# Performance work log

Measured on AMD Instinct MI355X. Metric: run time of the kernel, lower is better.

The kernel has to match this reference:

```python
import jax, jax.numpy as jnp
import numpy as np

N, L, D = 4, 2048, 1024
H_DIM, OUT_DIM = 1024, 1024


def setup_inputs() -> dict:
    key = jax.random.key(0)
    ks = jax.random.split(key, 7)
    scale = 0.02
    return {
        "x": jax.random.normal(ks[0], (N, L, D), dtype=jnp.float32),
        "Wq": jax.random.normal(ks[1], (D, H_DIM), dtype=jnp.float32) * scale,
        "bq": jnp.zeros((H_DIM,), dtype=jnp.float32),
        "Wk": jax.random.normal(ks[2], (D, H_DIM), dtype=jnp.float32) * scale,
        "bk": jnp.zeros((H_DIM,), dtype=jnp.float32),
        "Wv": jax.random.normal(ks[3], (D, OUT_DIM), dtype=jnp.float32) * scale,
        "bv": jnp.zeros((OUT_DIM,), dtype=jnp.float32),
    }


def reference(x, Wq, bq, Wk, bk, Wv, bv):
    # q,k: [N,L,h_dim], v: [N,L,out_dim]
    q = jnp.einsum("nld,dh->nlh", x, Wq) + bq
    k = jnp.einsum("nld,dh->nlh", x, Wk) + bk
    v = jnp.einsum("nld,do->nlo", x, Wv) + bv
    # scores: [N,L,L]
    qk = jnp.einsum("nlh,nmh->nlm", q, k)
    # NOTE: original scales by sqrt(qk.shape[-1]) == sqrt(L) (seq len), not sqrt(h_dim)
    seq_len = qk.shape[-1]
    s = jax.nn.softmax(qk / jnp.sqrt(jnp.asarray(seq_len, dtype=qk.dtype)), axis=-1)
    return jnp.einsum("nlm,nmo->nlo", s, v)
```

## Files before the change

### kernel.cpp

```cpp
#include <hip/hip_runtime.h>
#include <hip/hip_bf16.h>


typedef __attribute__((ext_vector_type(8))) short bf16x8;
typedef __attribute__((ext_vector_type(4))) float f32x4;

#define AS_G(p) ((__attribute__((address_space(1))) void*)(p))
#define AS_L(p) ((__attribute__((address_space(3))) void*)(p))

__device__ __forceinline__ unsigned short f2bf(float f) {
  unsigned int u = __float_as_uint(f);
  unsigned int lsb = (u >> 16) & 1u;
  u += 0x7fffu + lsb;
  return (unsigned short)(u >> 16);
}

__device__ __forceinline__ float bf2f(unsigned short h) {
  return __uint_as_float(((unsigned int)h) << 16);
}


template <int EPI>
__global__ __launch_bounds__(256) void gemm64(
    const unsigned short* __restrict__ A, const unsigned short* __restrict__ B,
    float* __restrict__ Cf, long long sA, long long sB, long long sC,
    int K, int lda, int ldb, int ldc,
    unsigned short* __restrict__ u0, unsigned short* __restrict__ u1,
    unsigned short* __restrict__ u2,
    const float* __restrict__ f0, const float* __restrict__ f1,
    const float* __restrict__ f2,
    float* __restrict__ rsum, float scale)
{
  __shared__ unsigned short lA[128 * 64];
  __shared__ unsigned short lB[128 * 64];

  const int t = threadIdx.x;
  const int rowBase = blockIdx.y * 128;
  const int colBase = blockIdx.x * 128;
  A += (long long)blockIdx.z * sA;
  B += (long long)blockIdx.z * sB;

  const int l = t & 63;
  const int w = t >> 6;
  const int wrow = (w >> 1) * 64;
  const int wcol = (w & 1) * 64;
  const int q = l >> 4;
  const int r16 = l & 15;

  f32x4 acc[4][4] = {};

  const int r0 = t >> 3;
  const int goff = (((t & 7) ^ (r0 & 7)) << 3);

  for (int kt = 0; kt < K; kt += 64) {
    __syncthreads();
#pragma unroll
    for (int u = 0; u < 4; u++) {
      const int row = r0 + 32 * u;
      __builtin_amdgcn_global_load_lds(AS_G(A + (size_t)(rowBase + row) * lda + kt + goff),
                                       AS_L(lA + (t + 256 * u) * 8), 16, 0, 0);
      __builtin_amdgcn_global_load_lds(AS_G(B + (size_t)(colBase + row) * ldb + kt + goff),
                                       AS_L(lB + (t + 256 * u) * 8), 16, 0, 0);
    }
    __syncthreads();

#pragma unroll
    for (int ks = 0; ks < 2; ks++) {
      bf16x8 af[4], bfr[4];
#pragma unroll
      for (int i = 0; i < 4; i++) {
        const int s = ((ks * 4 + q) ^ (r16 & 7));
        af[i] = *(const bf16x8*)(lA + (wrow + i * 16 + r16) * 64 + s * 8);
      }
#pragma unroll
      for (int j = 0; j < 4; j++) {
        const int s = ((ks * 4 + q) ^ (r16 & 7));
        bfr[j] = *(const bf16x8*)(lB + (wcol + j * 16 + r16) * 64 + s * 8);
      }
#pragma unroll
      for (int i = 0; i < 4; i++)
#pragma unroll
        for (int j = 0; j < 4; j++)
          acc[i][j] = __builtin_amdgcn_mfma_f32_16x16x32_bf16(af[i], bfr[j], acc[i][j], 0, 0, 0);
    }
  }

  if (EPI == 1) {
    unsigned short* p16 = u0 + (long long)blockIdx.z * sC;
    float* rs = rsum + (long long)blockIdx.z * 2048;
#pragma unroll
    for (int i = 0; i < 4; i++) {
#pragma unroll
      for (int r = 0; r < 4; r++) {
        int row = rowBase + wrow + i * 16 + q * 4 + r;
        float rowpart = 0.f;
#pragma unroll
        for (int j = 0; j < 4; j++) {
          int col = colBase + wcol + j * 16 + r16;
          float e = __expf(acc[i][j][r] * scale);
          p16[(size_t)row * ldc + col] = f2bf(e);
          rowpart += e;
        }
#pragma unroll
        for (int m = 1; m < 16; m <<= 1) rowpart += __shfl_xor(rowpart, m);
        if (r16 == 0) atomicAdd(rs + row, rowpart);
      }
    }
  } else if (EPI == 2) {
    const int seg = colBase >> 10;
    if (seg < 2) {
      unsigned short* dst = seg ? u1 : u0;
      const float* bias = seg ? f1 : f0;
      const int cb = colBase & 1023;
#pragma unroll
      for (int i = 0; i < 4; i++) {
#pragma unroll
        for (int r = 0; r < 4; r++) {
          int row = rowBase + wrow + i * 16 + q * 4 + r;
#pragma unroll
          for (int j = 0; j < 4; j++) {
            int col = cb + wcol + j * 16 + r16;
            dst[(size_t)row * 1024 + col] = f2bf(acc[i][j][r] + bias[col]);
          }
        }
      }
    } else {
      const int ob = colBase - 2048;
#pragma unroll
      for (int i = 0; i < 4; i++) {
        int posBase = rowBase + wrow + i * 16 + q * 4;
        int b = posBase >> 11;
        int pos = posBase & 2047;
#pragma unroll
        for (int j = 0; j < 4; j++) {
          int o = ob + wcol + j * 16 + r16;
          float bias = f2[o];
          ushort4 pk;
          pk.x = f2bf(acc[i][j][0] + bias);
          pk.y = f2bf(acc[i][j][1] + bias);
          pk.z = f2bf(acc[i][j][2] + bias);
          pk.w = f2bf(acc[i][j][3] + bias);
          *(ushort4*)(u2 + ((size_t)((b << 10) + o) * 2048 + pos)) = pk;
        }
      }
    }
  } else {
    float* C = Cf + (long long)blockIdx.z * sC;
    const float* rs = rsum + (long long)blockIdx.z * 2048;
#pragma unroll
    for (int i = 0; i < 4; i++) {
#pragma unroll
      for (int r = 0; r < 4; r++) {
        int row = rowBase + wrow + i * 16 + q * 4 + r;
        float inv = 1.0f / rs[row];
#pragma unroll
        for (int j = 0; j < 4; j++) {
          int col = colBase + wcol + j * 16 + r16;
          C[(size_t)row * ldc + col] = acc[i][j][r] * inv;
        }
      }
    }
  }
}


__global__ __launch_bounds__(256) void cast_f32_to_bf16(
    const float* __restrict__ in, unsigned short* __restrict__ out, int n4,
    float* __restrict__ rzero, int nz4)
{
  int i = blockIdx.x * 256 + threadIdx.x;
  if (i < nz4) ((float4*)rzero)[i] = make_float4(0.f, 0.f, 0.f, 0.f);
  if (i >= n4) return;
  float4 v = ((const float4*)in)[i];
  ushort4 o;
  o.x = f2bf(v.x); o.y = f2bf(v.y); o.z = f2bf(v.z); o.w = f2bf(v.w);
  ((ushort4*)out)[i] = o;
}


__global__ __launch_bounds__(256) void wtrans(
    const float* __restrict__ Wq, const float* __restrict__ Wk,
    const float* __restrict__ Wv, unsigned short* __restrict__ WT)
{
  __shared__ float tile[32][33];
  const float* in = blockIdx.z == 0 ? Wq : (blockIdx.z == 1 ? Wk : Wv);
  unsigned short* out = WT + (size_t)blockIdx.z * 1024 * 1024;
  const int bc = blockIdx.x * 32;
  const int br = blockIdx.y * 32;
  const int tx = threadIdx.x;
  const int ty = threadIdx.y;
#pragma unroll
  for (int i = 0; i < 4; i++)
    tile[ty + i * 8][tx] = in[(size_t)(br + ty + i * 8) * 1024 + bc + tx];
  __syncthreads();
#pragma unroll
  for (int i = 0; i < 4; i++)
    out[(size_t)(bc + ty + i * 8) * 1024 + br + tx] = f2bf(tile[tx][ty + i * 8]);
}


extern "C" void kernel_launch(void* const* d_in, const int* in_sizes, int n_in,
                              void* d_out, int out_size, void* d_ws, size_t ws_size,
                              hipStream_t stream) {
  (void)in_sizes; (void)n_in; (void)out_size;

  const float* x  = (const float*)d_in[0];
  const float* Wq = (const float*)d_in[1];
  const float* bq = (const float*)d_in[2];
  const float* Wk = (const float*)d_in[3];
  const float* bk = (const float*)d_in[4];
  const float* Wv = (const float*)d_in[5];
  const float* bv = (const float*)d_in[6];
  float* out = (float*)d_out;

  const int Nb = 4, L = 2048, D = 1024, H = 1024, O = 1024;
  const int M = Nb * L;
  const int NQKV = 3 * H;

  char* ws = (char*)d_ws;
  size_t off = 0;
  unsigned short* xb = (unsigned short*)(ws + off); off += (size_t)M * D * 2;
  unsigned short* qb = (unsigned short*)(ws + off); off += (size_t)M * H * 2;
  unsigned short* kb = (unsigned short*)(ws + off); off += (size_t)M * H * 2;
  unsigned short* vt = (unsigned short*)(ws + off); off += (size_t)M * O * 2;
  unsigned short* WT = (unsigned short*)(ws + off); off += (size_t)NQKV * D * 2;
  unsigned short* P  = (unsigned short*)(ws + off); off += (size_t)Nb * L * L * 2;
  float* rsum = (float*)(ws + off); off += (size_t)Nb * L * 4;
  if (ws_size < off) return;

  dim3 blk256(256);

  cast_f32_to_bf16<<<(M * D / 4 + 255) / 256, blk256, 0, stream>>>(
      x, xb, M * D / 4, rsum, Nb * L / 4);

  wtrans<<<dim3(32, 32, 3), dim3(32, 8), 0, stream>>>(Wq, Wk, Wv, WT);

  gemm64<2><<<dim3(NQKV / 128, M / 128, 1), blk256, 0, stream>>>(
      xb, WT, nullptr, 0, 0, 0, D, D, D, 0,
      qb, kb, vt, bq, bk, bv, nullptr, 0.f);

  gemm64<1><<<dim3(L / 128, L / 128, Nb), blk256, 0, stream>>>(
      qb, kb, nullptr, (long long)L * H, (long long)L * H, (long long)L * L,
      H, H, H, L,
      P, nullptr, nullptr, nullptr, nullptr, nullptr,
      rsum, 0.022097086912079608f );

  gemm64<3><<<dim3(O / 128, L / 128, Nb), blk256, 0, stream>>>(
      P, vt, out, (long long)L * L, (long long)O * L, (long long)L * O,
      L, L, L, O,
      nullptr, nullptr, nullptr, nullptr, nullptr, nullptr,
      rsum, 0.f);
}
```

Before: 264.1 us.

## Triple-buffer GEMM LDS loads and enlarge tiles to 256x128 with 512 threads

Replaces the single-buffered GEMM with a three-stage LDS pipeline that prefetches two K-tiles ahead using async global-to-LDS loads and vmcnt waits. Tiles grow to 256x128 per block with 8 waves, all fragment reads are hoisted before the MFMA burst, and wave priority is raised during the MFMAs. The aim is to hide global load latency and cut per-tile barrier stalls. In exchange it uses about 144KB of LDS per block, which limits occupancy, and it relies on correct manual waitcnt accounting.

```diff
diff --git a/kernel.cpp b/kernel.cpp
--- a/kernel.cpp
+++ b/kernel.cpp
@@ -15,13 +15,28 @@
   return (unsigned short)(u >> 16);
 }
 
-__device__ __forceinline__ float bf2f(unsigned short h) {
-  return __uint_as_float(((unsigned int)h) << 16);
-}
-
+#define WAITV(n) asm volatile("s_waitcnt vmcnt(" #n ")" ::: "memory")
+#define WAITL0   asm volatile("s_waitcnt lgkmcnt(0)" ::: "memory")
+#define BARRIER() do { __builtin_amdgcn_s_barrier(); asm volatile("" ::: "memory"); } while (0)
+
+
+#define STAGE(ktk, bb) do {                                                          \
+    unsigned short* dA_ = lds + (bb) * 24576;                                        \
+    unsigned short* dB_ = dA_ + 16384;                                               \
+    _Pragma("unroll")                                                                \
+    for (int u_ = 0; u_ < 4; u_++)                                                   \
+      __builtin_amdgcn_global_load_lds(                                              \
+          AS_G(A + (size_t)(rowBase + r0 + 64 * u_) * lda + (ktk) + goff),           \
+          AS_L(dA_ + ((size_t)t + 512 * u_) * 8), 16, 0, 0);                         \
+    _Pragma("unroll")                                                                \
+    for (int u_ = 0; u_ < 2; u_++)                                                   \
+      __builtin_amdgcn_global_load_lds(                                              \
+          AS_G(B + (size_t)(colBase + r0 + 64 * u_) * ldb + (ktk) + goff),           \
+          AS_L(dB_ + ((size_t)t + 512 * u_) * 8), 16, 0, 0);                         \
+  } while (0)
 
 template <int EPI>
-__global__ __launch_bounds__(256) void gemm64(
+__global__ __launch_bounds__(512, 2) void gemm_pipe(
     const unsigned short* __restrict__ A, const unsigned short* __restrict__ B,
     float* __restrict__ Cf, long long sA, long long sB, long long sC,
     int K, int lda, int ldb, int ldc,
@@ -31,11 +46,10 @@
     const float* __restrict__ f2,
     float* __restrict__ rsum, float scale)
 {
-  __shared__ unsigned short lA[128 * 64];
-  __shared__ unsigned short lB[128 * 64];
+  __shared__ unsigned short lds[3 * 24576];
 
   const int t = threadIdx.x;
-  const int rowBase = blockIdx.y * 128;
+  const int rowBase = blockIdx.y * 256;
   const int colBase = blockIdx.x * 128;
   A += (long long)blockIdx.z * sA;
   B += (long long)blockIdx.z * sB;
@@ -47,42 +61,55 @@
   const int q = l >> 4;
   const int r16 = l & 15;
 
+  const int r0 = t >> 3;
+  const int goff = ((t & 7) ^ (r0 & 7)) << 3;
+
   f32x4 acc[4][4] = {};
 
-  const int r0 = t >> 3;
-  const int goff = (((t & 7) ^ (r0 & 7)) << 3);
-
-  for (int kt = 0; kt < K; kt += 64) {
-    __syncthreads();
-#pragma unroll
-    for (int u = 0; u < 4; u++) {
-      const int row = r0 + 32 * u;
-      __builtin_amdgcn_global_load_lds(AS_G(A + (size_t)(rowBase + row) * lda + kt + goff),
-                                       AS_L(lA + (t + 256 * u) * 8), 16, 0, 0);
-      __builtin_amdgcn_global_load_lds(AS_G(B + (size_t)(colBase + row) * ldb + kt + goff),
-                                       AS_L(lB + (t + 256 * u) * 8), 16, 0, 0);
-    }
-    __syncthreads();
-
+  const int NT = K >> 6;
+
+  STAGE(0, 0);
+  STAGE(64, 1);
+
+  int cur = 0;
+  for (int it = 0; it < NT; ++it) {
+    const int kt = it << 6;
+    if (it + 2 < NT) {
+      int b2 = cur + 2; if (b2 >= 3) b2 -= 3;
+      STAGE(kt + 128, b2);
+      WAITV(12);
+    } else if (it + 1 < NT) {
+      WAITV(6);
+    } else {
+      WAITV(0);
+    }
+    BARRIER();
+
+    const unsigned short* bufA = lds + cur * 24576;
+    const unsigned short* bufB = bufA + 16384;
+    bf16x8 af[2][4], bfr[2][4];
 #pragma unroll
     for (int ks = 0; ks < 2; ks++) {
-      bf16x8 af[4], bfr[4];
-#pragma unroll
-      for (int i = 0; i < 4; i++) {
-        const int s = ((ks * 4 + q) ^ (r16 & 7));
-        af[i] = *(const bf16x8*)(lA + (wrow + i * 16 + r16) * 64 + s * 8);
-      }
-#pragma unroll
-      for (int j = 0; j < 4; j++) {
-        const int s = ((ks * 4 + q) ^ (r16 & 7));
-        bfr[j] = *(const bf16x8*)(lB + (wcol + j * 16 + r16) * 64 + s * 8);
-      }
+      const int s = (((ks * 4 + q) ^ (r16 & 7)) << 3);
 #pragma unroll
       for (int i = 0; i < 4; i++)
+        af[ks][i] = *(const bf16x8*)(bufA + (wrow + i * 16 + r16) * 64 + s);
+#pragma unroll
+      for (int j = 0; j < 4; j++)
+        bfr[ks][j] = *(const bf16x8*)(bufB + (wcol + j * 16 + r16) * 64 + s);
+    }
+    __builtin_amdgcn_s_setprio(1);
+#pragma unroll
+    for (int ks = 0; ks < 2; ks++)
+#pragma unroll
+      for (int i = 0; i < 4; i++)
 #pragma unroll
         for (int j = 0; j < 4; j++)
-          acc[i][j] = __builtin_amdgcn_mfma_f32_16x16x32_bf16(af[i], bfr[j], acc[i][j], 0, 0, 0);
-    }
+          acc[i][j] = __builtin_amdgcn_mfma_f32_16x16x32_bf16(af[ks][i], bfr[ks][j], acc[i][j], 0, 0, 0);
+    __builtin_amdgcn_s_setprio(0);
+    WAITL0;
+    BARRIER();
+    cur++; if (cur >= 3) cur -= 3;
   }
 
   if (EPI == 1) {
@@ -229,23 +256,24 @@
   if (ws_size < off) return;
 
   dim3 blk256(256);
+  dim3 blk512(512);
 
   cast_f32_to_bf16<<<(M * D / 4 + 255) / 256, blk256, 0, stream>>>(
       x, xb, M * D / 4, rsum, Nb * L / 4);
 
   wtrans<<<dim3(32, 32, 3), dim3(32, 8), 0, stream>>>(Wq, Wk, Wv, WT);
 
-  gemm64<2><<<dim3(NQKV / 128, M / 128, 1), blk256, 0, stream>>>(
+  gemm_pipe<2><<<dim3(NQKV / 128, M / 256, 1), blk512, 0, stream>>>(
       xb, WT, nullptr, 0, 0, 0, D, D, D, 0,
       qb, kb, vt, bq, bk, bv, nullptr, 0.f);
 
-  gemm64<1><<<dim3(L / 128, L / 128, Nb), blk256, 0, stream>>>(
+  gemm_pipe<1><<<dim3(L / 128, L / 256, Nb), blk512, 0, stream>>>(
       qb, kb, nullptr, (long long)L * H, (long long)L * H, (long long)L * L,
       H, H, H, L,
       P, nullptr, nullptr, nullptr, nullptr, nullptr,
       rsum, 0.022097086912079608f );
 
-  gemm64<3><<<dim3(O / 128, L / 128, Nb), blk256, 0, stream>>>(
+  gemm_pipe<3><<<dim3(O / 128, L / 256, Nb), blk512, 0, stream>>>(
       P, vt, out, (long long)L * L, (long long)O * L, (long long)L * O,
       L, L, L, O,
       nullptr, nullptr, nullptr, nullptr, nullptr, nullptr,
```

Result: no change. 261.3 us (-1.1%).

## Use 256x256 tiles with 8 waves and double-buffered LDS ping-pong GEMM

Applied to the files above, without the earlier changes.

Replaces the 128x128, 4-wave GEMM with a 256x256 tile computed by 8 waves, each producing 128x64. LDS is double-buffered so the global-to-LDS loads for the next K tile are issued in quarters between MFMA phases, with raised wave priority around the MFMA blocks. The goal is to hide load latency and raise data reuse per block. In exchange, each thread holds twice as many accumulators, LDS use grows to 128KB per block, and the grids shrink to fewer blocks, which may under-fill the 256 CUs on the smaller GEMMs.

```diff
diff --git a/kernel.cpp b/kernel.cpp
--- a/kernel.cpp
+++ b/kernel.cpp
@@ -15,13 +15,69 @@
   return (unsigned short)(u >> 16);
 }
 
-__device__ __forceinline__ float bf2f(unsigned short h) {
-  return __uint_as_float(((unsigned int)h) << 16);
-}
-
+#define WAITV0 asm volatile("s_waitcnt vmcnt(0)" ::: "memory")
+#define BARRIER() do { __builtin_amdgcn_s_barrier(); asm volatile("" ::: "memory"); } while (0)
+
+
+#define STAGE_A(ktk, h, bofs) do { _Pragma("unroll")                               \
+    for (int u_ = 0; u_ < 2; u_++)                                                 \
+      __builtin_amdgcn_global_load_lds(                                            \
+          AS_G(A + (size_t)(rowBase + (h) * 128 + u_ * 64 + r0) * lda + (ktk) + goff), \
+          AS_L(lds + (bofs) + ((h) * 128 + u_ * 64) * 64 + t * 8), 16, 0, 0);      \
+  } while (0)
+
+#define STAGE_B(ktk, h, bofs) do { _Pragma("unroll")                               \
+    for (int u_ = 0; u_ < 2; u_++)                                                 \
+      __builtin_amdgcn_global_load_lds(                                            \
+          AS_G(B + (size_t)(colBase + (h) * 128 + u_ * 64 + r0) * ldb + (ktk) + goff), \
+          AS_L(lds + (bofs) + 16384 + ((h) * 128 + u_ * 64) * 64 + t * 8), 16, 0, 0); \
+  } while (0)
+
+#define LOAD_A(ih, bofs) do { _Pragma("unroll")                                    \
+    for (int ks_ = 0; ks_ < 2; ks_++) { _Pragma("unroll")                          \
+      for (int ii = 0; ii < 4; ii++) {                                             \
+        int row_ = wrow + ((ih) * 4 + ii) * 16 + r16;                              \
+        int slot_ = (ks_ * 4 + q) ^ (r16 & 7);                                     \
+        af[ks_][ii] = *(const bf16x8*)(lds + (bofs) + row_ * 64 + slot_ * 8);      \
+      } } } while (0)
+
+#define LOAD_B(jh, bofs) do { _Pragma("unroll")                                    \
+    for (int ks_ = 0; ks_ < 2; ks_++) { _Pragma("unroll")                          \
+      for (int jj = 0; jj < 2; jj++) {                                             \
+        int row_ = wcol + ((jh) * 2 + jj) * 16 + r16;                              \
+        int slot_ = (ks_ * 4 + q) ^ (r16 & 7);                                     \
+        bfr[ks_][(jh) * 2 + jj] =                                                  \
+            *(const bf16x8*)(lds + (bofs) + 16384 + row_ * 64 + slot_ * 8);        \
+      } } } while (0)
+
+#define MM(ih, jh) do { __builtin_amdgcn_s_setprio(1); _Pragma("unroll")           \
+    for (int ks_ = 0; ks_ < 2; ks_++) { _Pragma("unroll")                          \
+      for (int ii = 0; ii < 4; ii++) { _Pragma("unroll")                           \
+        for (int jj = 0; jj < 2; jj++)                                             \
+          acc[(ih) * 4 + ii][(jh) * 2 + jj] =                                      \
+              __builtin_amdgcn_mfma_f32_16x16x32_bf16(                             \
+                  af[ks_][ii], bfr[ks_][(jh) * 2 + jj],                            \
+                  acc[(ih) * 4 + ii][(jh) * 2 + jj], 0, 0, 0);                     \
+      } }                                                                          \
+    __builtin_amdgcn_s_setprio(0); } while (0)
+
+#define KTILE(ktk, bofs, obofs, doStage) do {                                      \
+                                                                 \
+    LOAD_A(0, bofs); LOAD_B(0, bofs);                                              \
+    if (doStage) { STAGE_B((ktk) + 64, 1, obofs); STAGE_A((ktk) + 64, 0, obofs); } \
+    BARRIER(); MM(0, 0); BARRIER();                                                \
+                                                                 \
+    LOAD_B(1, bofs);                                                               \
+    if (doStage) { STAGE_A((ktk) + 64, 1, obofs); STAGE_B((ktk) + 64, 0, obofs); } \
+    BARRIER(); MM(0, 1); BARRIER();                                                \
+                                                                 \
+    LOAD_A(1, bofs);                                                               \
+    BARRIER(); MM(1, 1); BARRIER();                                                \
+                                    \
+    MM(1, 0); WAITV0; BARRIER(); } while (0)
 
 template <int EPI>
-__global__ __launch_bounds__(256) void gemm64(
+__global__ __launch_bounds__(512, 2) void gemm_8p(
     const unsigned short* __restrict__ A, const unsigned short* __restrict__ B,
     float* __restrict__ Cf, long long sA, long long sB, long long sC,
     int K, int lda, int ldb, int ldc,
@@ -31,65 +87,43 @@
     const float* __restrict__ f2,
     float* __restrict__ rsum, float scale)
 {
-  __shared__ unsigned short lA[128 * 64];
-  __shared__ unsigned short lB[128 * 64];
+  __shared__ unsigned short lds[2 * 32768];
 
   const int t = threadIdx.x;
-  const int rowBase = blockIdx.y * 128;
-  const int colBase = blockIdx.x * 128;
+  const int rowBase = blockIdx.y * 256;
+  const int colBase = blockIdx.x * 256;
   A += (long long)blockIdx.z * sA;
   B += (long long)blockIdx.z * sB;
 
   const int l = t & 63;
   const int w = t >> 6;
-  const int wrow = (w >> 1) * 64;
-  const int wcol = (w & 1) * 64;
+  const int wrow = (w >> 2) * 128;
+  const int wcol = (w & 3) * 64;
   const int q = l >> 4;
   const int r16 = l & 15;
 
-  f32x4 acc[4][4] = {};
-
   const int r0 = t >> 3;
-  const int goff = (((t & 7) ^ (r0 & 7)) << 3);
-
-  for (int kt = 0; kt < K; kt += 64) {
-    __syncthreads();
-#pragma unroll
-    for (int u = 0; u < 4; u++) {
-      const int row = r0 + 32 * u;
-      __builtin_amdgcn_global_load_lds(AS_G(A + (size_t)(rowBase + row) * lda + kt + goff),
-                                       AS_L(lA + (t + 256 * u) * 8), 16, 0, 0);
-      __builtin_amdgcn_global_load_lds(AS_G(B + (size_t)(colBase + row) * ldb + kt + goff),
-                                       AS_L(lB + (t + 256 * u) * 8), 16, 0, 0);
-    }
-    __syncthreads();
-
-#pragma unroll
-    for (int ks = 0; ks < 2; ks++) {
-      bf16x8 af[4], bfr[4];
-#pragma unroll
-      for (int i = 0; i < 4; i++) {
-        const int s = ((ks * 4 + q) ^ (r16 & 7));
-        af[i] = *(const bf16x8*)(lA + (wrow + i * 16 + r16) * 64 + s * 8);
-      }
-#pragma unroll
-      for (int j = 0; j < 4; j++) {
-        const int s = ((ks * 4 + q) ^ (r16 & 7));
-        bfr[j] = *(const bf16x8*)(lB + (wcol + j * 16 + r16) * 64 + s * 8);
-      }
-#pragma unroll
-      for (int i = 0; i < 4; i++)
-#pragma unroll
-        for (int j = 0; j < 4; j++)
-          acc[i][j] = __builtin_amdgcn_mfma_f32_16x16x32_bf16(af[i], bfr[j], acc[i][j], 0, 0, 0);
-    }
+  const int goff = ((t & 7) ^ (r0 & 7)) << 3;
+
+  f32x4 acc[8][4] = {};
+  bf16x8 af[2][4], bfr[2][4];
+
+  const int NT = K >> 6;
+
+  STAGE_A(0, 0, 0); STAGE_A(0, 1, 0);
+  STAGE_B(0, 0, 0); STAGE_B(0, 1, 0);
+  WAITV0; BARRIER();
+
+  for (int kt2 = 0; kt2 < NT; kt2 += 2) {
+    KTILE(kt2 * 64, 0, 32768, true);
+    KTILE(kt2 * 64 + 64, 32768, 0, kt2 + 2 < NT);
   }
 
   if (EPI == 1) {
     unsigned short* p16 = u0 + (long long)blockIdx.z * sC;
     float* rs = rsum + (long long)blockIdx.z * 2048;
 #pragma unroll
-    for (int i = 0; i < 4; i++) {
+    for (int i = 0; i < 8; i++) {
 #pragma unroll
       for (int r = 0; r < 4; r++) {
         int row = rowBase + wrow + i * 16 + q * 4 + r;
@@ -113,7 +147,7 @@
       const float* bias = seg ? f1 : f0;
       const int cb = colBase & 1023;
 #pragma unroll
-      for (int i = 0; i < 4; i++) {
+      for (int i = 0; i < 8; i++) {
 #pragma unroll
         for (int r = 0; r < 4; r++) {
           int row = rowBase + wrow + i * 16 + q * 4 + r;
@@ -127,7 +161,7 @@
     } else {
       const int ob = colBase - 2048;
 #pragma unroll
-      for (int i = 0; i < 4; i++) {
+      for (int i = 0; i < 8; i++) {
         int posBase = rowBase + wrow + i * 16 + q * 4;
         int b = posBase >> 11;
         int pos = posBase & 2047;
@@ -148,7 +182,7 @@
     float* C = Cf + (long long)blockIdx.z * sC;
     const float* rs = rsum + (long long)blockIdx.z * 2048;
 #pragma unroll
-    for (int i = 0; i < 4; i++) {
+    for (int i = 0; i < 8; i++) {
 #pragma unroll
       for (int r = 0; r < 4; r++) {
         int row = rowBase + wrow + i * 16 + q * 4 + r;
@@ -229,23 +263,24 @@
   if (ws_size < off) return;
 
   dim3 blk256(256);
+  dim3 blk512(512);
 
   cast_f32_to_bf16<<<(M * D / 4 + 255) / 256, blk256, 0, stream>>>(
       x, xb, M * D / 4, rsum, Nb * L / 4);
 
   wtrans<<<dim3(32, 32, 3), dim3(32, 8), 0, stream>>>(Wq, Wk, Wv, WT);
 
-  gemm64<2><<<dim3(NQKV / 128, M / 128, 1), blk256, 0, stream>>>(
+  gemm_8p<2><<<dim3(NQKV / 256, M / 256, 1), blk512, 0, stream>>>(
       xb, WT, nullptr, 0, 0, 0, D, D, D, 0,
       qb, kb, vt, bq, bk, bv, nullptr, 0.f);
 
-  gemm64<1><<<dim3(L / 128, L / 128, Nb), blk256, 0, stream>>>(
+  gemm_8p<1><<<dim3(L / 256, L / 256, Nb), blk512, 0, stream>>>(
       qb, kb, nullptr, (long long)L * H, (long long)L * H, (long long)L * L,
       H, H, H, L,
       P, nullptr, nullptr, nullptr, nullptr, nullptr,
       rsum, 0.022097086912079608f );
 
-  gemm64<3><<<dim3(O / 128, L / 128, Nb), blk256, 0, stream>>>(
+  gemm_8p<3><<<dim3(O / 256, L / 256, Nb), blk512, 0, stream>>>(
       P, vt, out, (long long)L * L, (long long)O * L, (long long)L * O,
       L, L, L, O,
       nullptr, nullptr, nullptr, nullptr, nullptr, nullptr,
```

Result: no change. 259.4 us (-1.8%).

## Triple-buffer LDS with async prefetch in 256x128 GEMM tiles using 512 threads

Applied to the files above, without the earlier changes.

Replaces the single-buffered, two-barrier GEMM loop with a three-stage LDS ring: global_load_lds for tile k+2 is issued while MFMAs run on tile k, and completion is tracked with explicit vmcnt waits and raw barriers. Block tiles grow to 256x128 with 8 waves (512 threads), and the MFMA section runs at raised wave priority. The aim is to hide global-memory latency and cut barrier stalls, at the cost of 144KB of LDS per block and fragile hand-written waitcnt accounting.

```diff
diff --git a/kernel.cpp b/kernel.cpp
--- a/kernel.cpp
+++ b/kernel.cpp
@@ -15,13 +15,48 @@
   return (unsigned short)(u >> 16);
 }
 
-__device__ __forceinline__ float bf2f(unsigned short h) {
-  return __uint_as_float(((unsigned int)h) << 16);
-}
-
+#define WAITV(n) asm volatile("s_waitcnt vmcnt(" #n ")" ::: "memory")
+#define BAR() do { asm volatile("" ::: "memory");                             \
+    __builtin_amdgcn_s_barrier();                                             \
+    asm volatile("" ::: "memory"); } while (0)
+
+
+#define BUFE 24576
+
+#define S64A(ktk, rb, bofs)                                                   \
+  __builtin_amdgcn_global_load_lds(                                           \
+      AS_G(A + (size_t)(rowBase + (rb) * 64 + r0) * lda + (ktk) + goff),      \
+      AS_L(lds + (bofs) + (rb) * 4096 + t * 8), 16, 0, 0)
+
+#define S64B(ktk, rb, bofs)                                                   \
+  __builtin_amdgcn_global_load_lds(                                           \
+      AS_G(B + (size_t)(colBase + (rb) * 64 + r0) * ldb + (ktk) + goff),      \
+      AS_L(lds + (bofs) + 16384 + (rb) * 4096 + t * 8), 16, 0, 0)
+
+#define LDA(bofs, ks_) do { _Pragma("unroll")                                 \
+    for (int ii = 0; ii < 4; ii++) {                                          \
+      int row_ = wrow + ii * 16 + r16;                                        \
+      int slot_ = ((ks_) * 4 + q) ^ (r16 & 7);                                \
+      af[ii] = *(const bf16x8*)(lds + (bofs) + row_ * 64 + slot_ * 8);        \
+    } } while (0)
+
+#define LDB(bofs, ks_) do { _Pragma("unroll")                                 \
+    for (int jj = 0; jj < 4; jj++) {                                          \
+      int row_ = wcol + jj * 16 + r16;                                        \
+      int slot_ = ((ks_) * 4 + q) ^ (r16 & 7);                                \
+      bfr[jj] = *(const bf16x8*)(lds + (bofs) + 16384 + row_ * 64 + slot_ * 8); \
+    } } while (0)
+
+#define MMK() do { __builtin_amdgcn_s_setprio(1); _Pragma("unroll")           \
+    for (int ii = 0; ii < 4; ii++) { _Pragma("unroll")                        \
+      for (int jj = 0; jj < 4; jj++)                                          \
+        acc[ii][jj] = __builtin_amdgcn_mfma_f32_16x16x32_bf16(                \
+            af[ii], bfr[jj], acc[ii][jj], 0, 0, 0);                           \
+    }                                                                         \
+    __builtin_amdgcn_s_setprio(0); } while (0)
 
 template <int EPI>
-__global__ __launch_bounds__(256) void gemm64(
+__global__ __launch_bounds__(512, 2) void gemm_fp(
     const unsigned short* __restrict__ A, const unsigned short* __restrict__ B,
     float* __restrict__ Cf, long long sA, long long sB, long long sC,
     int K, int lda, int ldb, int ldc,
@@ -31,11 +66,10 @@
     const float* __restrict__ f2,
     float* __restrict__ rsum, float scale)
 {
-  __shared__ unsigned short lA[128 * 64];
-  __shared__ unsigned short lB[128 * 64];
+  __shared__ unsigned short lds[3 * BUFE];
 
   const int t = threadIdx.x;
-  const int rowBase = blockIdx.y * 128;
+  const int rowBase = blockIdx.y * 256;
   const int colBase = blockIdx.x * 128;
   A += (long long)blockIdx.z * sA;
   B += (long long)blockIdx.z * sB;
@@ -47,42 +81,34 @@
   const int q = l >> 4;
   const int r16 = l & 15;
 
+  const int r0 = t >> 3;
+  const int goff = ((t & 7) ^ (r0 & 7)) << 3;
+
   f32x4 acc[4][4] = {};
-
-  const int r0 = t >> 3;
-  const int goff = (((t & 7) ^ (r0 & 7)) << 3);
-
+  bf16x8 af[4], bfr[4];
+
+  S64A(0, 0, 0); S64A(0, 1, 0); S64A(0, 2, 0); S64A(0, 3, 0);
+  S64B(0, 0, 0); S64B(0, 1, 0);
+  S64A(64, 0, BUFE); S64A(64, 1, BUFE); S64A(64, 2, BUFE); S64A(64, 3, BUFE);
+  S64B(64, 0, BUFE); S64B(64, 1, BUFE);
+  WAITV(6);
+  BAR();
+
+  int bo = 0, bn1 = BUFE, bn2 = 2 * BUFE;
   for (int kt = 0; kt < K; kt += 64) {
-    __syncthreads();
-#pragma unroll
-    for (int u = 0; u < 4; u++) {
-      const int row = r0 + 32 * u;
-      __builtin_amdgcn_global_load_lds(AS_G(A + (size_t)(rowBase + row) * lda + kt + goff),
-                                       AS_L(lA + (t + 256 * u) * 8), 16, 0, 0);
-      __builtin_amdgcn_global_load_lds(AS_G(B + (size_t)(colBase + row) * ldb + kt + goff),
-                                       AS_L(lB + (t + 256 * u) * 8), 16, 0, 0);
-    }
-    __syncthreads();
-
-#pragma unroll
-    for (int ks = 0; ks < 2; ks++) {
-      bf16x8 af[4], bfr[4];
-#pragma unroll
-      for (int i = 0; i < 4; i++) {
-        const int s = ((ks * 4 + q) ^ (r16 & 7));
-        af[i] = *(const bf16x8*)(lA + (wrow + i * 16 + r16) * 64 + s * 8);
-      }
-#pragma unroll
-      for (int j = 0; j < 4; j++) {
-        const int s = ((ks * 4 + q) ^ (r16 & 7));
-        bfr[j] = *(const bf16x8*)(lB + (wcol + j * 16 + r16) * 64 + s * 8);
-      }
-#pragma unroll
-      for (int i = 0; i < 4; i++)
-#pragma unroll
-        for (int j = 0; j < 4; j++)
-          acc[i][j] = __builtin_amdgcn_mfma_f32_16x16x32_bf16(af[i], bfr[j], acc[i][j], 0, 0, 0);
-    }
+    const bool st = (kt + 128 < K);
+    LDA(bo, 0); LDB(bo, 0);
+    if (st) { S64A(kt + 128, 0, bn2); S64A(kt + 128, 1, bn2); S64B(kt + 128, 0, bn2); }
+    BAR();
+    MMK();
+    BAR();
+    LDA(bo, 1); LDB(bo, 1);
+    if (st) { S64A(kt + 128, 2, bn2); S64A(kt + 128, 3, bn2); S64B(kt + 128, 1, bn2); }
+    BAR();
+    MMK();
+    if (st) { WAITV(6); } else { WAITV(0); }
+    BAR();
+    int tmp = bo; bo = bn1; bn1 = bn2; bn2 = tmp;
   }
 
   if (EPI == 1) {
@@ -229,23 +255,24 @@
   if (ws_size < off) return;
 
   dim3 blk256(256);
+  dim3 blk512(512);
 
   cast_f32_to_bf16<<<(M * D / 4 + 255) / 256, blk256, 0, stream>>>(
       x, xb, M * D / 4, rsum, Nb * L / 4);
 
   wtrans<<<dim3(32, 32, 3), dim3(32, 8), 0, stream>>>(Wq, Wk, Wv, WT);
 
-  gemm64<2><<<dim3(NQKV / 128, M / 128, 1), blk256, 0, stream>>>(
+  gemm_fp<2><<<dim3(NQKV / 128, M / 256, 1), blk512, 0, stream>>>(
       xb, WT, nullptr, 0, 0, 0, D, D, D, 0,
       qb, kb, vt, bq, bk, bv, nullptr, 0.f);
 
-  gemm64<1><<<dim3(L / 128, L / 128, Nb), blk256, 0, stream>>>(
+  gemm_fp<1><<<dim3(L / 128, L / 256, Nb), blk512, 0, stream>>>(
       qb, kb, nullptr, (long long)L * H, (long long)L * H, (long long)L * L,
       H, H, H, L,
       P, nullptr, nullptr, nullptr, nullptr, nullptr,
       rsum, 0.022097086912079608f );
 
-  gemm64<3><<<dim3(O / 128, L / 128, Nb), blk256, 0, stream>>>(
+  gemm_fp<3><<<dim3(O / 128, L / 256, Nb), blk512, 0, stream>>>(
       P, vt, out, (long long)L * L, (long long)O * L, (long long)L * O,
       L, L, L, O,
       nullptr, nullptr, nullptr, nullptr, nullptr, nullptr,
```

Measured after the change: 259.7 us. Within noise of the previous version (-1.7%).
